# Optimization experiments

Measured on AMD Instinct MI355X. Metric: run time of the kernel, lower is better.

## Reference

```python
import jax, jax.numpy as jnp
import numpy as np


def setup_inputs() -> dict:
    key = jax.random.key(0)
    gramBatch = jax.random.normal(key, (8, 8, 1024, 16, 16), dtype=jnp.float32)
    return {"gramBatch": gramBatch, "patchPerRow": 32}


def reference(gramBatch, patchPerRow):
    # Parallel (parralelMode=True) path of GramDistMap.forward.
    B, C, N, D1, D2 = gramBatch.shape
    g = gramBatch.reshape(B, C, N, D1 * D2)            # [B,C,N,D]
    # gramNorm = sqrt(sum((g*g)^2)) = sqrt(sum(g^4))
    g2 = g * g
    norm = jnp.sqrt(jnp.sum(g2 * g2, axis=-1))         # [B,C,N]
    # sum_d (g_i - g_j)^2 = ||g_i||^2 + ||g_j||^2 - 2 g_i . g_j,
    # computed without materializing the [B,C,N,N,D] broadcast tensor.
    sq = jnp.sum(g2, axis=-1)                          # [B,C,N]
    dots = jnp.einsum('bcnd,bcmd->bcnm', g, g)         # [B,C,N,N]
    dist2 = sq[..., :, None] + sq[..., None, :] - 2.0 * dots
    distMat = dist2 / (norm[..., :, None] * norm[..., None, :])
    return distMat.mean(axis=1)                        # [B,N,N]
```

## Files before the change

### kernel.cpp

```cpp
#include <hip/hip_runtime.h>
#include <stdint.h>

#define NB 8
#define NC 8
#define NN 1024
#define ND 256
#define KK 2048
#define BM 128
#define BN 64
#define BKK 64
#define NT (KK / BKK)

typedef float f32x4 __attribute__((ext_vector_type(4)));
typedef short bf16x8 __attribute__((ext_vector_type(8)));

__device__ __forceinline__ unsigned short f2bf(float x) {
  union { float f; uint32_t u; } a; a.f = x;
  uint32_t u = a.u;
  return (unsigned short)((u + 0x7FFFu + ((u >> 16) & 1u)) >> 16);
}

__device__ __forceinline__ void gload16(const void* g, void* l) {
  __builtin_amdgcn_global_load_lds(
      (__attribute__((address_space(1))) uint32_t*)g,
      (__attribute__((address_space(3))) uint32_t*)l, 16, 0, 0);
}

__global__ __launch_bounds__(256) void prep_kernel(
    const float* __restrict__ g, unsigned short* __restrict__ ghat,
    float* __restrict__ uFlat, float* __restrict__ vFlat) {
  int tid = threadIdx.x;
  int wave = tid >> 6, lane = tid & 63;
  int sub = lane & 15, grp = lane >> 4;
  int rowid = (blockIdx.x * 4 + wave) * 4 + grp;
  const float* row = g + (size_t)rowid * ND;
  f32x4 v[4];
  float s2 = 0.f, s4 = 0.f;
#pragma unroll
  for (int q = 0; q < 4; ++q) {
    v[q] = *(const f32x4*)(row + q * 64 + sub * 4);
#pragma unroll
    for (int e = 0; e < 4; ++e) { float x2 = v[q][e] * v[q][e]; s2 += x2; s4 += x2 * x2; }
  }
#pragma unroll
  for (int off = 8; off; off >>= 1) {
    s2 += __shfl_xor(s2, off);
    s4 += __shfl_xor(s4, off);
  }
  float rn = rsqrtf(s4);
  int n = rowid & (NN - 1);
  int bc = rowid >> 10;
  int c = bc & (NC - 1);
  int b = bc >> 3;
  unsigned short* dst = ghat + ((size_t)(b * NN + n)) * KK + (size_t)c * ND + sub * 4;
#pragma unroll
  for (int q = 0; q < 4; ++q) {
    ushort4 o;
    o.x = f2bf(v[q][0] * rn); o.y = f2bf(v[q][1] * rn);
    o.z = f2bf(v[q][2] * rn); o.w = f2bf(v[q][3] * rn);
    *(ushort4*)(dst + q * 64) = o;
  }
  if (sub == 0) { uFlat[rowid] = s2 * rn; vFlat[rowid] = rn; }
}

__global__ __launch_bounds__(256) void gram_gemm_kernel(
    const unsigned short* __restrict__ ghat,
    const float* __restrict__ uFlat, const float* __restrict__ vFlat,
    float* __restrict__ out) {
  __shared__ union {
    struct { unsigned short A[3][BM * BKK]; unsigned short Bt[3][BN * BKK]; } s;
    struct { float R[128][16]; float Cc[64][16]; } e;
  } sm;

  int bid = blockIdx.x;
  int logical = (bid & 7) * 128 + (bid >> 3);
  int b = logical >> 7;
  int t7 = logical & 127;
  int row0 = (t7 >> 4) * BM;
  int col0 = (t7 & 15) * BN;
  int tid = threadIdx.x;
  int lane = tid & 63;
  int wave = tid >> 6;
  int wr = (wave >> 1) * 64;
  int wc = (wave & 1) * 32;

  const unsigned short* gA = ghat + (size_t)(b * NN + row0) * KK;
  const unsigned short* gB = ghat + (size_t)(b * NN + col0) * KK;

  f32x4 acc[4][2];
#pragma unroll
  for (int i = 0; i < 4; ++i)
#pragma unroll
    for (int j = 0; j < 2; ++j)
      acc[i][j] = f32x4{0.f, 0.f, 0.f, 0.f};

  int rsel = lane & 15;
  int khalf = lane >> 4;
  int r8 = tid >> 3;
  int s8 = tid & 7;

  auto STAGE = [&](int t, int bi) {
    int k0 = t * BKK;
#pragma unroll
    for (int i = 0; i < 4; ++i) {
      int rr = i * 32 + r8;
      int sg = s8 ^ (rr & 7);
      gload16(gA + (size_t)rr * KK + k0 + sg * 8, &sm.s.A[bi][rr * BKK + s8 * 8]);
    }
#pragma unroll
    for (int i = 0; i < 2; ++i) {
      int rr = i * 32 + r8;
      int sg = s8 ^ (rr & 7);
      gload16(gB + (size_t)rr * KK + k0 + sg * 8, &sm.s.Bt[bi][rr * BKK + s8 * 8]);
    }
  };

  STAGE(0, 0);
  STAGE(1, 1);

  int cidx = 0;
  for (int t = 0; t < NT; ++t) {
    if (t + 1 < NT) {
      asm volatile("s_waitcnt vmcnt(6)" ::: "memory");
    } else {
      asm volatile("s_waitcnt vmcnt(0)" ::: "memory");
    }
    __builtin_amdgcn_sched_barrier(0);
    __builtin_amdgcn_s_barrier();
    __builtin_amdgcn_sched_barrier(0);

    if (t + 2 < NT) {
      int pidx = cidx ? cidx - 1 : 2;
      STAGE(t + 2, pidx);
    }

    __builtin_amdgcn_s_setprio(1);
#pragma unroll
    for (int kk = 0; kk < 2; ++kk) {
      bf16x8 af[4], bfb[2];
#pragma unroll
      for (int i = 0; i < 4; ++i) {
        int rr = wr + i * 16 + rsel;
        int slot = (kk * 4 + khalf) ^ (rr & 7);
        af[i] = *(const bf16x8*)&sm.s.A[cidx][rr * BKK + slot * 8];
      }
#pragma unroll
      for (int j = 0; j < 2; ++j) {
        int rr = wc + j * 16 + rsel;
        int slot = (kk * 4 + khalf) ^ (rr & 7);
        bfb[j] = *(const bf16x8*)&sm.s.Bt[cidx][rr * BKK + slot * 8];
      }
#pragma unroll
      for (int i = 0; i < 4; ++i)
#pragma unroll
        for (int j = 0; j < 2; ++j)
          acc[i][j] = __builtin_amdgcn_mfma_f32_16x16x32_bf16(af[i], bfb[j], acc[i][j], 0, 0, 0);
    }
    __builtin_amdgcn_s_setprio(0);

    cidx = (cidx == 2) ? 0 : cidx + 1;
  }
  __syncthreads();

  {
    int rl = tid >> 1;
    int half = tid & 1;
    const float* src = half ? vFlat : uFlat;
#pragma unroll
    for (int c = 0; c < 8; ++c)
      sm.e.R[rl][half * 8 + c] = src[(size_t)(b * NC + c) * NN + row0 + rl];
    if (rl < 64) {
#pragma unroll
      for (int c = 0; c < 8; ++c)
        sm.e.Cc[rl][half * 8 + c] = src[(size_t)(b * NC + c) * NN + col0 + rl];
    }
  }
  __syncthreads();

  int lr = (lane >> 4) * 4;
  int lc = lane & 15;
#pragma unroll
  for (int j = 0; j < 2; ++j) {
    int cl = wc + j * 16 + lc;
    f32x4 uc0 = *(const f32x4*)&sm.e.Cc[cl][0];
    f32x4 uc1 = *(const f32x4*)&sm.e.Cc[cl][4];
    f32x4 vc0 = *(const f32x4*)&sm.e.Cc[cl][8];
    f32x4 vc1 = *(const f32x4*)&sm.e.Cc[cl][12];
#pragma unroll
    for (int i = 0; i < 4; ++i) {
#pragma unroll
      for (int q = 0; q < 4; ++q) {
        int rl = wr + i * 16 + lr + q;
        f32x4 r0 = *(const f32x4*)&sm.e.R[rl][0];
        f32x4 r1 = *(const f32x4*)&sm.e.R[rl][4];
        f32x4 r2 = *(const f32x4*)&sm.e.R[rl][8];
        f32x4 r3 = *(const f32x4*)&sm.e.R[rl][12];
        float fr = r0[0]*vc0[0]+r0[1]*vc0[1]+r0[2]*vc0[2]+r0[3]*vc0[3]
                 + r1[0]*vc1[0]+r1[1]*vc1[1]+r1[2]*vc1[2]+r1[3]*vc1[3]
                 + r2[0]*uc0[0]+r2[1]*uc0[1]+r2[2]*uc0[2]+r2[3]*uc0[3]
                 + r3[0]*uc1[0]+r3[1]*uc1[1]+r3[2]*uc1[2]+r3[3]*uc1[3];
        float val = 0.125f * fr - 0.25f * acc[i][j][q];
        out[((size_t)(b * NN + row0 + rl)) * NN + (size_t)(col0 + cl)] = val;
      }
    }
  }
}

extern "C" void kernel_launch(void* const* d_in, const int* in_sizes, int n_in,
                              void* d_out, int out_size, void* d_ws, size_t ws_size,
                              hipStream_t stream) {
  const float* g = (const float*)d_in[0];
  unsigned short* ghat = (unsigned short*)d_ws;
  float* uFlat = (float*)((char*)d_ws + (size_t)NB * NN * KK * 2);
  float* vFlat = uFlat + (size_t)NB * NC * NN;
  float* outp = (float*)d_out;

  prep_kernel<<<NB * NC * NN / 16, 256, 0, stream>>>(g, ghat, uFlat, vFlat);
  gram_gemm_kernel<<<1024, 256, 0, stream>>>(ghat, uFlat, vFlat, outp);
}
```

Measured before the change: 216.5 us.

## Load MFMA operands directly from global memory, dropping LDS staging pipeline

Replaces the triple-buffered LDS staging (global_load_lds with swizzle, waitcnt and barriers) with per-wave direct global loads of bf16 fragments into registers, unrolled by two. This removes the LDS traffic and the block-wide barrier each K step. In exchange, waves sharing rows now issue redundant global/L2 loads, the loads are uncoalesced 16-byte row strided accesses, and latency hiding depends on the compiler and on occupancy.

```diff
diff --git a/kernel.cpp b/kernel.cpp
--- a/kernel.cpp
+++ b/kernel.cpp
@@ -18,12 +18,6 @@
   union { float f; uint32_t u; } a; a.f = x;
   uint32_t u = a.u;
   return (unsigned short)((u + 0x7FFFu + ((u >> 16) & 1u)) >> 16);
-}
-
-__device__ __forceinline__ void gload16(const void* g, void* l) {
-  __builtin_amdgcn_global_load_lds(
-      (__attribute__((address_space(1))) uint32_t*)g,
-      (__attribute__((address_space(3))) uint32_t*)l, 16, 0, 0);
 }
 
 __global__ __launch_bounds__(256) void prep_kernel(
@@ -67,10 +61,7 @@
     const unsigned short* __restrict__ ghat,
     const float* __restrict__ uFlat, const float* __restrict__ vFlat,
     float* __restrict__ out) {
-  __shared__ union {
-    struct { unsigned short A[3][BM * BKK]; unsigned short Bt[3][BN * BKK]; } s;
-    struct { float R[128][16]; float Cc[64][16]; } e;
-  } sm;
+  __shared__ struct { float R[128][16]; float Cc[64][16]; } sm;
 
   int bid = blockIdx.x;
   int logical = (bid & 7) * 128 + (bid >> 3);
@@ -84,8 +75,13 @@
   int wr = (wave >> 1) * 64;
   int wc = (wave & 1) * 32;
 
-  const unsigned short* gA = ghat + (size_t)(b * NN + row0) * KK;
-  const unsigned short* gB = ghat + (size_t)(b * NN + col0) * KK;
+  int rsel = lane & 15;
+  int khalf = lane >> 4;
+
+  const unsigned short* baseA =
+      ghat + (size_t)(b * NN + row0 + wr + rsel) * KK + khalf * 8;
+  const unsigned short* baseB =
+      ghat + (size_t)(b * NN + col0 + wc + rsel) * KK + khalf * 8;
 
   f32x4 acc[4][2];
 #pragma unroll
@@ -94,73 +90,27 @@
     for (int j = 0; j < 2; ++j)
       acc[i][j] = f32x4{0.f, 0.f, 0.f, 0.f};
 
-  int rsel = lane & 15;
-  int khalf = lane >> 4;
-  int r8 = tid >> 3;
-  int s8 = tid & 7;
-
-  auto STAGE = [&](int t, int bi) {
+#pragma unroll 2
+  for (int t = 0; t < NT; ++t) {
     int k0 = t * BKK;
+    bf16x8 af[4][2], bfb[2][2];
 #pragma unroll
-    for (int i = 0; i < 4; ++i) {
-      int rr = i * 32 + r8;
-      int sg = s8 ^ (rr & 7);
-      gload16(gA + (size_t)rr * KK + k0 + sg * 8, &sm.s.A[bi][rr * BKK + s8 * 8]);
+    for (int kk = 0; kk < 2; ++kk) {
+#pragma unroll
+      for (int i = 0; i < 4; ++i)
+        af[i][kk] = *(const bf16x8*)(baseA + (size_t)i * 16 * KK + k0 + kk * 32);
+#pragma unroll
+      for (int j = 0; j < 2; ++j)
+        bfb[j][kk] = *(const bf16x8*)(baseB + (size_t)j * 16 * KK + k0 + kk * 32);
     }
 #pragma unroll
-    for (int i = 0; i < 2; ++i) {
-      int rr = i * 32 + r8;
-      int sg = s8 ^ (rr & 7);
-      gload16(gB + (size_t)rr * KK + k0 + sg * 8, &sm.s.Bt[bi][rr * BKK + s8 * 8]);
-    }
-  };
-
-  STAGE(0, 0);
-  STAGE(1, 1);
-
-  int cidx = 0;
-  for (int t = 0; t < NT; ++t) {
-    if (t + 1 < NT) {
-      asm volatile("s_waitcnt vmcnt(6)" ::: "memory");
-    } else {
-      asm volatile("s_waitcnt vmcnt(0)" ::: "memory");
-    }
-    __builtin_amdgcn_sched_barrier(0);
-    __builtin_amdgcn_s_barrier();
-    __builtin_amdgcn_sched_barrier(0);
-
-    if (t + 2 < NT) {
-      int pidx = cidx ? cidx - 1 : 2;
-      STAGE(t + 2, pidx);
-    }
-
-    __builtin_amdgcn_s_setprio(1);
-#pragma unroll
-    for (int kk = 0; kk < 2; ++kk) {
-      bf16x8 af[4], bfb[2];
-#pragma unroll
-      for (int i = 0; i < 4; ++i) {
-        int rr = wr + i * 16 + rsel;
-        int slot = (kk * 4 + khalf) ^ (rr & 7);
-        af[i] = *(const bf16x8*)&sm.s.A[cidx][rr * BKK + slot * 8];
-      }
-#pragma unroll
-      for (int j = 0; j < 2; ++j) {
-        int rr = wc + j * 16 + rsel;
-        int slot = (kk * 4 + khalf) ^ (rr & 7);
-        bfb[j] = *(const bf16x8*)&sm.s.Bt[cidx][rr * BKK + slot * 8];
-      }
+    for (int kk = 0; kk < 2; ++kk)
 #pragma unroll
       for (int i = 0; i < 4; ++i)
 #pragma unroll
         for (int j = 0; j < 2; ++j)
-          acc[i][j] = __builtin_amdgcn_mfma_f32_16x16x32_bf16(af[i], bfb[j], acc[i][j], 0, 0, 0);
-    }
-    __builtin_amdgcn_s_setprio(0);
-
-    cidx = (cidx == 2) ? 0 : cidx + 1;
+          acc[i][j] = __builtin_amdgcn_mfma_f32_16x16x32_bf16(af[i][kk], bfb[j][kk], acc[i][j], 0, 0, 0);
   }
-  __syncthreads();
 
   {
     int rl = tid >> 1;
@@ -168,11 +118,11 @@
     const float* src = half ? vFlat : uFlat;
 #pragma unroll
     for (int c = 0; c < 8; ++c)
-      sm.e.R[rl][half * 8 + c] = src[(size_t)(b * NC + c) * NN + row0 + rl];
+      sm.R[rl][half * 8 + c] = src[(size_t)(b * NC + c) * NN + row0 + rl];
     if (rl < 64) {
 #pragma unroll
       for (int c = 0; c < 8; ++c)
-        sm.e.Cc[rl][half * 8 + c] = src[(size_t)(b * NC + c) * NN + col0 + rl];
+        sm.Cc[rl][half * 8 + c] = src[(size_t)(b * NC + c) * NN + col0 + rl];
     }
   }
   __syncthreads();
@@ -182,19 +132,19 @@
 #pragma unroll
   for (int j = 0; j < 2; ++j) {
     int cl = wc + j * 16 + lc;
-    f32x4 uc0 = *(const f32x4*)&sm.e.Cc[cl][0];
-    f32x4 uc1 = *(const f32x4*)&sm.e.Cc[cl][4];
-    f32x4 vc0 = *(const f32x4*)&sm.e.Cc[cl][8];
-    f32x4 vc1 = *(const f32x4*)&sm.e.Cc[cl][12];
+    f32x4 uc0 = *(const f32x4*)&sm.Cc[cl][0];
+    f32x4 uc1 = *(const f32x4*)&sm.Cc[cl][4];
+    f32x4 vc0 = *(const f32x4*)&sm.Cc[cl][8];
+    f32x4 vc1 = *(const f32x4*)&sm.Cc[cl][12];
 #pragma unroll
     for (int i = 0; i < 4; ++i) {
 #pragma unroll
       for (int q = 0; q < 4; ++q) {
         int rl = wr + i * 16 + lr + q;
-        f32x4 r0 = *(const f32x4*)&sm.e.R[rl][0];
-        f32x4 r1 = *(const f32x4*)&sm.e.R[rl][4];
-        f32x4 r2 = *(const f32x4*)&sm.e.R[rl][8];
-        f32x4 r3 = *(const f32x4*)&sm.e.R[rl][12];
+        f32x4 r0 = *(const f32x4*)&sm.R[rl][0];
+        f32x4 r1 = *(const f32x4*)&sm.R[rl][4];
+        f32x4 r2 = *(const f32x4*)&sm.R[rl][8];
+        f32x4 r3 = *(const f32x4*)&sm.R[rl][12];
         float fr = r0[0]*vc0[0]+r0[1]*vc0[1]+r0[2]*vc0[2]+r0[3]*vc0[3]
                  + r1[0]*vc1[0]+r1[1]*vc1[1]+r1[2]*vc1[2]+r1[3]*vc1[3]
                  + r2[0]*uc0[0]+r2[1]*uc0[1]+r2[2]*uc0[2]+r2[3]*uc0[3]
```

New measurement: 288.8 us. 1.33x slower.
